# Kernel tuning notes

Hardware: AMD Instinct MI355X
Metric: run time of the kernel (lower is better)

## Reference

```python
import jax, jax.numpy as jnp
import numpy as np

GROUPS = 32
EPS = 1e-5


def group_norm(x, gamma, beta):
    # x: [b, h, w, c] NHWC; normalize over (h, w, c/GROUPS) within each group
    b, h, w, c = x.shape
    xg = x.reshape(b, h, w, GROUPS, c // GROUPS)
    mean = jnp.mean(xg, axis=(1, 2, 4), keepdims=True)
    var = jnp.var(xg, axis=(1, 2, 4), keepdims=True)
    xg = (xg - mean) * jax.lax.rsqrt(var + EPS)
    return xg.reshape(b, h, w, c) * gamma + beta


def setup_inputs() -> dict:
    key = jax.random.key(0)
    ks = jax.random.split(key, 6)
    c = 512
    s = 1.0 / np.sqrt(c)  # fan-in scaled init for conv weights
    return {
        "x": jax.random.normal(ks[0], (2, 64, 64, c), dtype=jnp.float32),
        "gamma": jnp.ones((c,), jnp.float32),
        "beta": jnp.zeros((c,), jnp.float32),
        "wq": jax.random.normal(ks[1], (c, c), jnp.float32) * s,
        "bq": jnp.zeros((c,), jnp.float32),
        "wk": jax.random.normal(ks[2], (c, c), jnp.float32) * s,
        "bk": jnp.zeros((c,), jnp.float32),
        "wv": jax.random.normal(ks[3], (c, c), jnp.float32) * s,
        "bv": jnp.zeros((c,), jnp.float32),
        "wo": jax.random.normal(ks[4], (c, c), jnp.float32) * s,
        "bo": jnp.zeros((c,), jnp.float32),
    }


def reference(x, gamma, beta, wq, bq, wk, bk, wv, bv, wo, bo):
    b, h, w, c = x.shape
    n = h * w
    hn = group_norm(x, gamma, beta)
    hn = hn.reshape(b, n, c)  # flatten spatial -> tokens
    # 1x1 convs == pointwise linear
    q = hn @ wq + bq  # [b, n, c]
    k = hn @ wk + bk
    v = hn @ wv + bv
    scores = jnp.einsum("bic,bjc->bij", q, k) * (c ** -0.5)  # [b, n, n]
    attn = jax.nn.softmax(scores, axis=-1)
    out = jnp.einsum("bij,bjc->bic", attn, v)  # [b, n, c]
    out = out @ wo + bo
    return x + out.reshape(b, h, w, c)
```

## Files before the change

### kernel.cpp

```cpp
#include <hip/hip_runtime.h>
#include <hip/hip_fp8.h>
#include <stdint.h>


typedef unsigned short u16;
typedef unsigned char u8;
typedef short s16x8 __attribute__((ext_vector_type(8)));
typedef float f32x4 __attribute__((ext_vector_type(4)));
typedef int i32x8 __attribute__((ext_vector_type(8)));
typedef float f32x16 __attribute__((ext_vector_type(16)));

#define NTOK 4096
#define CH   512

__device__ inline u16 f2bf(float f) {
  union { float f; uint32_t u; } v; v.f = f;
  uint32_t r = v.u + 0x7FFFu + ((v.u >> 16) & 1u);
  return (u16)(r >> 16);
}
__device__ inline float bf2f(u16 b) {
  union { uint32_t u; float f; } v; v.u = (uint32_t)b << 16; return v.f;
}
__device__ inline f32x4 mfma16(s16x8 a, s16x8 b, f32x4 c) {
  return __builtin_amdgcn_mfma_f32_16x16x32_bf16(a, b, c, 0, 0, 0);
}
__device__ inline f32x16 mfma_mx8(i32x8 a, i32x8 b, f32x16 c) {
  return __builtin_amdgcn_mfma_scale_f32_32x32x64_f8f6f4(
      a, b, c, 0 , 0 ,
      0, 0x7F7F7F7F, 0, 0x7F7F7F7F);
}
__device__ inline uint32_t pk_fp8x4(float e0, float e1, float e2, float e3) {
#if __has_builtin(__builtin_amdgcn_cvt_pk_fp8_f32)
  int v = __builtin_amdgcn_cvt_pk_fp8_f32(e0, e1, 0, false);
  v = __builtin_amdgcn_cvt_pk_fp8_f32(e2, e3, v, true);
  return (uint32_t)v;
#else
  __hip_fp8_e4m3 a(e0), b(e1), c(e2), d(e3);
  return (uint32_t)*(u8*)&a | ((uint32_t)*(u8*)&b << 8) |
         ((uint32_t)*(u8*)&c << 16) | ((uint32_t)*(u8*)&d << 24);
#endif
}
__device__ inline u8 f2fp8(float x) {
#if __has_builtin(__builtin_amdgcn_cvt_pk_fp8_f32)
  int v = __builtin_amdgcn_cvt_pk_fp8_f32(x, x, 0, false);
  return (u8)(v & 0xFF);
#else
  __hip_fp8_e4m3 h(x); return *(u8*)&h;
#endif
}
__device__ inline void gload_lds16(const void* g, void* l) {
  __builtin_amdgcn_global_load_lds(
      (const __attribute__((address_space(1))) unsigned*)g,
      (__attribute__((address_space(3))) unsigned*)l, 16, 0, 0);
}
__device__ inline uint4 addbf8(uint4 a, uint4 b) {
  union { uint4 v; u16 h[8]; } A, B, O; A.v = a; B.v = b;
#pragma unroll
  for (int j = 0; j < 8; j++) O.h[j] = f2bf(bf2f(A.h[j]) + bf2f(B.h[j]));
  return O.v;
}

__global__ __launch_bounds__(256) void gn_stats_kernel(
    const float* __restrict__ x, float* __restrict__ part) {
  int c = blockIdx.x, b = blockIdx.y;
  int t = threadIdx.x, g = t & 31;
  const float* xb = x + (size_t)b * NTOK * CH + (size_t)c * 64 * CH + g * 16;
  float s = 0.f, q = 0.f;
  for (int p = 0; p < 8; p++) {
    const float* ptr = xb + ((size_t)p * 8 + (t >> 5)) * CH;
#pragma unroll
    for (int j = 0; j < 4; j++) {
      float4 v = *(const float4*)(ptr + j * 4);
      s += v.x + v.y + v.z + v.w;
      q += v.x * v.x + v.y * v.y + v.z * v.z + v.w * v.w;
    }
  }
  __shared__ float ls[32][8], lq[32][8];
  ls[g][t >> 5] = s; lq[g][t >> 5] = q;
  __syncthreads();
  if (t < 32) {
    float S = 0.f, Q = 0.f;
#pragma unroll
    for (int j = 0; j < 8; j++) { S += ls[t][j]; Q += lq[t][j]; }
    float2 o; o.x = S; o.y = Q;
    *(float2*)&part[(((size_t)b * 64 + c) * 32 + t) * 2] = o;
  }
}

__global__ __launch_bounds__(256) void gn_apply_kernel(
    const float* __restrict__ x, const float* __restrict__ part,
    const float* __restrict__ gamma, const float* __restrict__ beta,
    u16* __restrict__ hn) {
  int blk = blockIdx.x, b = blk >> 9, t = threadIdx.x;
  __shared__ float msh[32], rsh[32];
  if (t < 64) {
    int g = t >> 1, half = t & 1;
    float S = 0.f, Q = 0.f;
    for (int c = half * 32; c < half * 32 + 32; c++) {
      float2 p = *(const float2*)&part[(((size_t)b * 64 + c) * 32 + g) * 2];
      S += p.x; Q += p.y;
    }
    S += __shfl_xor(S, 1, 64);
    Q += __shfl_xor(Q, 1, 64);
    if (half == 0) {
      float mean = S * (1.f / 65536.f);
      float var = Q * (1.f / 65536.f) - mean * mean;
      msh[g] = mean; rsh[g] = rsqrtf(var + 1e-5f);
    }
  }
  __syncthreads();
  size_t base = (size_t)b * NTOK * CH + (size_t)(blk & 511) * 4096 + t * 16;
  int ch0 = (t * 16) & 511;
  float mean = msh[t & 31], rstd = rsh[t & 31];
  const float* xp = x + base;
  union { u16 h[16]; uint4 v[2]; } o;
#pragma unroll
  for (int j = 0; j < 4; j++) {
    float4 xv = *(const float4*)(xp + j * 4);
    float4 gv = *(const float4*)(gamma + ch0 + j * 4);
    float4 bv = *(const float4*)(beta + ch0 + j * 4);
    o.h[j * 4 + 0] = f2bf((xv.x - mean) * rstd * gv.x + bv.x);
    o.h[j * 4 + 1] = f2bf((xv.y - mean) * rstd * gv.y + bv.y);
    o.h[j * 4 + 2] = f2bf((xv.z - mean) * rstd * gv.z + bv.z);
    o.h[j * 4 + 3] = f2bf((xv.w - mean) * rstd * gv.w + bv.w);
  }
  *(uint4*)(hn + base) = o.v[0];
  *(uint4*)(hn + base + 8) = o.v[1];
}

__global__ __launch_bounds__(256) void wprep_kernel(
    const float* w0, const float* w1, const float* w2, const float* w3,
    u16* t0, u16* t1, u16* t2, u16* t3) {
  int z = blockIdx.z;
  const float* w = z == 0 ? w0 : z == 1 ? w1 : z == 2 ? w2 : w3;
  u16* wt = z == 0 ? t0 : z == 1 ? t1 : z == 2 ? t2 : t3;
  __shared__ float tile[32][33];
  int k0 = blockIdx.x * 32, n0 = blockIdx.y * 32;
  int tx = threadIdx.x & 31, ty = threadIdx.x >> 5;
  for (int r = 0; r < 4; r++)
    tile[ty * 4 + r][tx] = w[(size_t)(k0 + ty * 4 + r) * CH + n0 + tx];
  __syncthreads();
  for (int r = 0; r < 4; r++)
    wt[(size_t)(n0 + ty * 4 + r) * CH + k0 + tx] = f2bf(tile[tx][ty * 4 + r]);
}

__global__ __launch_bounds__(256, 2) void qkv_gemm_kernel(
    const u16* __restrict__ A, const u16* __restrict__ Wcat,
    const float* __restrict__ bq, const float* __restrict__ bk,
    const float* __restrict__ bvv, u8* __restrict__ qf8, u8* __restrict__ kf8,
    u8* __restrict__ vtf8) {
  __shared__ __align__(16) u8 pool[65536];
  int m0 = blockIdx.x * 128, n0 = blockIdx.y * 128;
  int t = threadIdx.x, lane = t & 63, wave = t >> 6;
  int wx = wave & 1, wy = wave >> 1;
  int lane4 = lane >> 4;
  f32x4 acc[4][4] = {};
  const u16 *Asrc[4], *Bsrc[4];
  int dsto[4];
#pragma unroll
  for (int j = 0; j < 4; j++) {
    int u = t + j * 256, row = u >> 3, ch = (u & 7) ^ (row & 7);
    Asrc[j] = A + (size_t)(m0 + row) * CH + ch * 8;
    Bsrc[j] = Wcat + (size_t)(n0 + row) * CH + ch * 8;
    dsto[j] = u * 16;
  }
#pragma unroll
  for (int j = 0; j < 4; j++) {
    gload_lds16(Asrc[j], pool + dsto[j]);
    gload_lds16(Bsrc[j], pool + 32768 + dsto[j]);
  }
  __syncthreads();
  for (int kt = 0; kt < 8; kt++) {
    int co = (kt & 1) * 16384;
    const u16* Ac = (const u16*)(pool + co);
    const u16* Bc = (const u16*)(pool + 32768 + co);
    if (kt < 7) {
      int no = ((kt & 1) ^ 1) * 16384;
#pragma unroll
      for (int j = 0; j < 4; j++) {
        Asrc[j] += 64; Bsrc[j] += 64;
        gload_lds16(Asrc[j], pool + no + dsto[j]);
        gload_lds16(Bsrc[j], pool + 32768 + no + dsto[j]);
      }
    }
    __builtin_amdgcn_s_setprio(1);
#pragma unroll
    for (int ks = 0; ks < 2; ks++) {
      int kc = ks * 4 + lane4;
      s16x8 af[4], bf[4];
#pragma unroll
      for (int i = 0; i < 4; i++) {
        int ra = wx * 64 + i * 16 + (lane & 15);
        af[i] = *(const s16x8*)&Ac[ra * 64 + ((kc ^ (ra & 7)) << 3)];
        int rb = wy * 64 + i * 16 + (lane & 15);
        bf[i] = *(const s16x8*)&Bc[rb * 64 + ((kc ^ (rb & 7)) << 3)];
      }
#pragma unroll
      for (int mi = 0; mi < 4; mi++)
#pragma unroll
        for (int ni = 0; ni < 4; ni++)
          acc[mi][ni] = mfma16(af[mi], bf[ni], acc[mi][ni]);
    }
    __builtin_amdgcn_s_setprio(0);
    __syncthreads();
  }
  int proj = n0 >> 9;
  int r0l = wx * 64 + lane4 * 4;
  if (proj <= 1) {
    u8* O = proj == 0 ? qf8 : kf8;
    const float* bias = proj == 0 ? bq : bk;
#pragma unroll
    for (int mi = 0; mi < 4; mi++)
#pragma unroll
      for (int ni = 0; ni < 4; ni++) {
        int colp = (n0 & 511) + wy * 64 + ni * 16 + (lane & 15);
        float bv = bias[colp];
#pragma unroll
        for (int r = 0; r < 4; r++)
          O[(size_t)(m0 + r0l + mi * 16 + r) * CH + colp] =
              f2fp8(acc[mi][ni][r] + bv);
      }
  } else {
#pragma unroll
    for (int mi = 0; mi < 4; mi++)
#pragma unroll
      for (int ni = 0; ni < 4; ni++) {
        int colp = (n0 & 511) + wy * 64 + ni * 16 + (lane & 15);
        float bv = bvv[colp];
        int row = m0 + r0l + mi * 16;
        int bb = row >> 12, nn = row & 4095;
        uint32_t p = pk_fp8x4(acc[mi][ni][0] + bv, acc[mi][ni][1] + bv,
                              acc[mi][ni][2] + bv, acc[mi][ni][3] + bv);
        *(uint32_t*)&vtf8[((size_t)bb * CH + colp) * NTOK + nn] = p;
      }
  }
}

__global__ __launch_bounds__(256) void gemm_out_kernel(
    const u16* __restrict__ A, const u16* __restrict__ A2,
    const u16* __restrict__ Wt, const float* __restrict__ bias,
    float* __restrict__ out, const float* __restrict__ xres) {
  __shared__ __align__(16) u16 As[128 * 40];
  __shared__ __align__(16) u16 Bs[64 * 40];
  int m0 = blockIdx.x * 128, n0 = blockIdx.y * 64;
  int t = threadIdx.x, lane = t & 63, wave = t >> 6;
  int wm = wave >> 1, wn = wave & 1;
  f32x4 acc[4][2] = {};
  int arow = t >> 2, ac = t & 3;
  size_t aoff = (size_t)(m0 + arow) * CH + ac * 8;
  const u16* Bg = Wt + (size_t)(n0 + arow) * CH + ac * 8;
  uint4 a0 = addbf8(*(const uint4*)(A + aoff), *(const uint4*)(A2 + aoff));
  uint4 a1 = addbf8(*(const uint4*)(A + aoff + 64 * CH),
                    *(const uint4*)(A2 + aoff + 64 * CH));
  uint4 b0 = *(const uint4*)Bg;
  for (int kt = 0; kt < 16; kt++) {
    __syncthreads();
    *(uint4*)&As[(size_t)arow * 40 + ac * 8] = a0;
    *(uint4*)&As[(size_t)(arow + 64) * 40 + ac * 8] = a1;
    *(uint4*)&Bs[(size_t)arow * 40 + ac * 8] = b0;
    if (kt < 15) {
      aoff += 32; Bg += 32;
      a0 = addbf8(*(const uint4*)(A + aoff), *(const uint4*)(A2 + aoff));
      a1 = addbf8(*(const uint4*)(A + aoff + 64 * CH),
                  *(const uint4*)(A2 + aoff + 64 * CH));
      b0 = *(const uint4*)Bg;
    }
    __syncthreads();
    s16x8 af[4], bfr[2];
#pragma unroll
    for (int i = 0; i < 4; i++)
      af[i] = *(const s16x8*)&As[(wm * 64 + i * 16 + (lane & 15)) * 40 + (lane >> 4) * 8];
#pragma unroll
    for (int j = 0; j < 2; j++)
      bfr[j] = *(const s16x8*)&Bs[(wn * 32 + j * 16 + (lane & 15)) * 40 + (lane >> 4) * 8];
    __builtin_amdgcn_s_setprio(1);
#pragma unroll
    for (int mi = 0; mi < 4; mi++)
#pragma unroll
      for (int ni = 0; ni < 2; ni++)
        acc[mi][ni] = mfma16(af[mi], bfr[ni], acc[mi][ni]);
    __builtin_amdgcn_s_setprio(0);
  }
  int r0l = wm * 64 + ((lane >> 4) * 4);
  int c0l = wn * 32 + (lane & 15);
#pragma unroll
  for (int mi = 0; mi < 4; mi++)
#pragma unroll
    for (int ni = 0; ni < 2; ni++) {
      int col = n0 + c0l + ni * 16;
      float bv = bias[col];
#pragma unroll
      for (int r = 0; r < 4; r++) {
        size_t idx = (size_t)(m0 + r0l + mi * 16 + r) * CH + col;
        out[idx] = xres[idx] + acc[mi][ni][r] + bv;
      }
    }
}

__global__ __launch_bounds__(256, 2) void s_gemm_kernel(
    const u8* __restrict__ qf8, const u8* __restrict__ kf8,
    u8* __restrict__ S, float* __restrict__ lpart) {
  const float QS = 0.044194173824159216f;
  __shared__ __align__(16) u8 pool[65536];
  int bz = blockIdx.z;
  const u8* qb = qf8 + (size_t)bz * NTOK * CH;
  const u8* kb = kf8 + (size_t)bz * NTOK * CH;
  u8* Sg = S + (size_t)bz * NTOK * NTOK;
  float* lp = lpart + (size_t)bz * 64 * NTOK;
  int m0 = blockIdx.x * 128, n0 = blockIdx.y * 128;
  int t = threadIdx.x, lane = t & 63, wave = t >> 6;
  int wmx = wave & 1, wy = wave >> 1;
  int lh = lane >> 5;
  f32x16 acc[2][2] = {};
  const u8 *Asrc[4], *Bsrc[4];
  int dsto[4];
#pragma unroll
  for (int j = 0; j < 4; j++) {
    int u = t + j * 256, row = u >> 3, ch = (u & 7) ^ (row & 7);
    Asrc[j] = kb + (size_t)(n0 + row) * CH + ch * 16;
    Bsrc[j] = qb + (size_t)(m0 + row) * CH + ch * 16;
    dsto[j] = u * 16;
  }
#pragma unroll
  for (int j = 0; j < 4; j++) {
    gload_lds16(Asrc[j], pool + dsto[j]);
    gload_lds16(Bsrc[j], pool + 32768 + dsto[j]);
  }
  __syncthreads();
  for (int kt = 0; kt < 4; kt++) {
    int co = (kt & 1) * 16384;
    const u8* Ac = pool + co;
    const u8* Bc = pool + 32768 + co;
    if (kt < 3) {
      int no = ((kt & 1) ^ 1) * 16384;
#pragma unroll
      for (int j = 0; j < 4; j++) {
        Asrc[j] += 128; Bsrc[j] += 128;
        gload_lds16(Asrc[j], pool + no + dsto[j]);
        gload_lds16(Bsrc[j], pool + 32768 + no + dsto[j]);
      }
    }
    __builtin_amdgcn_s_setprio(1);
#pragma unroll
    for (int kh = 0; kh < 2; kh++) {
      int cb = kh * 4 + lh * 2;
      union { i32x8 v; uint4 qq[2]; } bu[2];
#pragma unroll
      for (int bj = 0; bj < 2; bj++) {
        int rb = wmx * 64 + bj * 32 + (lane & 31);
        const u8* bp = &Bc[rb * 128];
        bu[bj].qq[0] = *(const uint4*)&bp[(cb ^ (rb & 7)) << 4];
        bu[bj].qq[1] = *(const uint4*)&bp[((cb + 1) ^ (rb & 7)) << 4];
      }
#pragma unroll
      for (int ai = 0; ai < 2; ai++) {
        int ra = wy * 64 + ai * 32 + (lane & 31);
        union { i32x8 v; uint4 qq[2]; } au;
        const u8* ap = &Ac[ra * 128];
        au.qq[0] = *(const uint4*)&ap[(cb ^ (ra & 7)) << 4];
        au.qq[1] = *(const uint4*)&ap[((cb + 1) ^ (ra & 7)) << 4];
#pragma unroll
        for (int bj = 0; bj < 2; bj++)
          acc[ai][bj] = mfma_mx8(au.v, bu[bj].v, acc[ai][bj]);
      }
    }
    __builtin_amdgcn_s_setprio(0);
    __syncthreads();
  }
  uint32_t* Stile = (uint32_t*)pool;
  float psum[2] = {};
#pragma unroll
  for (int ai = 0; ai < 2; ai++) {
#pragma unroll
    for (int bj = 0; bj < 2; bj++) {
      int ml = wmx * 64 + bj * 32 + (lane & 31);
#pragma unroll
      for (int qd = 0; qd < 4; qd++) {
        float e0 = __expf(acc[ai][bj][qd * 4 + 0] * QS);
        float e1 = __expf(acc[ai][bj][qd * 4 + 1] * QS);
        float e2 = __expf(acc[ai][bj][qd * 4 + 2] * QS);
        float e3 = __expf(acc[ai][bj][qd * 4 + 3] * QS);
        psum[bj] += e0 + e1 + e2 + e3;
        int nw = wy * 16 + ai * 8 + qd * 2 + lh;
        Stile[ml * 32 + (nw ^ ((ml & 7) << 2))] = pk_fp8x4(e0, e1, e2, e3);
      }
    }
  }
#pragma unroll
  for (int bj = 0; bj < 2; bj++) {
    float v = psum[bj];
    v += __shfl_xor(v, 32, 64);
    if (lane < 32) {
      int m = m0 + wmx * 64 + bj * 32 + lane;
      lp[(size_t)((n0 >> 6) + wy) * NTOK + m] = v;
    }
  }
  __syncthreads();
#pragma unroll
  for (int p = 0; p < 4; p++) {
    int row = (t >> 3) + p * 32;
    int g = t & 7;
    int w0 = (g * 4) ^ ((row & 7) << 2);
    uint4 v;
    v.x = Stile[row * 32 + w0 + 0];
    v.y = Stile[row * 32 + w0 + 1];
    v.z = Stile[row * 32 + w0 + 2];
    v.w = Stile[row * 32 + w0 + 3];
    *(uint4*)&Sg[(size_t)(m0 + row) * NTOK + n0 + g * 16] = v;
  }
}

__global__ __launch_bounds__(256) void lreduce_kernel(
    const float* __restrict__ lpart, float* __restrict__ linv) {
  int b = blockIdx.y;
  int row = blockIdx.x * 256 + threadIdx.x;
  const float* lp = lpart + (size_t)b * 64 * NTOK + row;
  float s = 0.f;
#pragma unroll
  for (int c = 0; c < 64; c++) s += lp[(size_t)c * NTOK];
  linv[b * NTOK + row] = 1.f / s;
}

__global__ __launch_bounds__(512) void pv_gemm_kernel(
    const u8* __restrict__ S, const u8* __restrict__ vtf8,
    const float* __restrict__ linv, u16* __restrict__ part0,
    u16* __restrict__ part1) {
  __shared__ __align__(16) u8 Asw[2][128 * 128];
  __shared__ __align__(16) u8 Bsw[2][128 * 128];
  int flat = blockIdx.x + 32 * blockIdx.y + 128 * blockIdx.z;
  int xcd = flat & 7, u = flat >> 3;
  int m_t = xcd * 4 + (u & 3);
  int n_i = (u >> 2) & 3;
  int spb = u >> 4, sp = spb & 1, b = spb >> 1;
  int m0 = m_t * 128, n0 = n_i * 128, kbase = sp * 2048;
  const u8* Sb = S + (size_t)b * NTOK * NTOK;
  const u8* vb = vtf8 + (size_t)b * CH * NTOK;
  int t = threadIdx.x, lane = t & 63, wave = t >> 6;
  int wm = wave >> 2, wn = wave & 3;
  int lh = lane >> 5;
  f32x16 acc[2] = {};
  const u8 *Asrc[2], *Bsrc[2];
  int uoff[2];
#pragma unroll
  for (int j = 0; j < 2; j++) {
    int uu = t + j * 512, row = uu >> 3, ch = (uu & 7) ^ (row & 7);
    Asrc[j] = Sb + (size_t)(m0 + row) * NTOK + kbase + ch * 16;
    Bsrc[j] = vb + (size_t)(n0 + row) * NTOK + kbase + ch * 16;
    uoff[j] = uu * 16;
  }
#pragma unroll
  for (int j = 0; j < 2; j++) {
    gload_lds16(Asrc[j], &Asw[0][uoff[j]]); gload_lds16(Bsrc[j], &Bsw[0][uoff[j]]);
  }
  __syncthreads();
  int cur = 0;
  int rb = wn * 32 + (lane & 31);
  for (int kt = 0; kt < 16; kt++) {
    if (kt < 15) {
#pragma unroll
      for (int j = 0; j < 2; j++) {
        Asrc[j] += 128; Bsrc[j] += 128;
        gload_lds16(Asrc[j], &Asw[cur ^ 1][uoff[j]]);
        gload_lds16(Bsrc[j], &Bsw[cur ^ 1][uoff[j]]);
      }
    }
    __builtin_amdgcn_s_setprio(1);
#pragma unroll
    for (int kh = 0; kh < 2; kh++) {
      int cb = kh * 4 + lh * 2;
      union { i32x8 v; uint4 qq[2]; } bu;
      const u8* bp = &Bsw[cur][rb * 128];
      bu.qq[0] = *(const uint4*)&bp[(cb ^ (rb & 7)) << 4];
      bu.qq[1] = *(const uint4*)&bp[((cb + 1) ^ (rb & 7)) << 4];
#pragma unroll
      for (int mi = 0; mi < 2; mi++) {
        int ra = wm * 64 + mi * 32 + (lane & 31);
        union { i32x8 v; uint4 qq[2]; } au;
        const u8* ap = &Asw[cur][ra * 128];
        au.qq[0] = *(const uint4*)&ap[(cb ^ (ra & 7)) << 4];
        au.qq[1] = *(const uint4*)&ap[((cb + 1) ^ (ra & 7)) << 4];
        acc[mi] = mfma_mx8(au.v, bu.v, acc[mi]);
      }
    }
    __builtin_amdgcn_s_setprio(0);
    __syncthreads();
    cur ^= 1;
  }
  u16* Od = (sp ? part1 : part0) + (size_t)b * NTOK * CH;
  const float* lv = linv + (size_t)b * NTOK;
#pragma unroll
  for (int mi = 0; mi < 2; mi++)
#pragma unroll
    for (int reg = 0; reg < 16; reg++) {
      int crow = (reg & 3) + 8 * (reg >> 2) + 4 * lh;
      int gr = wm * 64 + mi * 32 + crow;
      float inv = lv[m0 + gr];
      Od[(size_t)(m0 + gr) * CH + n0 + wn * 32 + (lane & 31)] =
          f2bf(acc[mi][reg] * inv);
    }
}

extern "C" void kernel_launch(void* const* d_in, const int* in_sizes, int n_in,
                              void* d_out, int out_size, void* d_ws, size_t ws_size,
                              hipStream_t stream) {
  const float* x     = (const float*)d_in[0];
  const float* gamma = (const float*)d_in[1];
  const float* beta  = (const float*)d_in[2];
  const float* wq    = (const float*)d_in[3];
  const float* bq    = (const float*)d_in[4];
  const float* wk    = (const float*)d_in[5];
  const float* bk    = (const float*)d_in[6];
  const float* wv    = (const float*)d_in[7];
  const float* bv    = (const float*)d_in[8];
  const float* wo    = (const float*)d_in[9];
  const float* bo    = (const float*)d_in[10];

  char* ws = (char*)d_ws;
  u16* hn   = (u16*)(ws + 0);
  u16* q    = (u16*)(ws + 8388608);
  u8*  vtf8 = (u8*)(ws + 25165824);
  u16* wqt  = (u16*)(ws + 33554432);
  u16* wkt  = (u16*)(ws + 34078720);
  u16* wvt  = (u16*)(ws + 34603008);
  u16* wot  = (u16*)(ws + 35127296);
  u8*  S    = (u8*)(ws + 35651584);
  float* lpart = (float*)(ws + 71303168);
  float* linv  = (float*)(ws + 73400320);
  u8*  qf8  = (u8*)(ws + 75497472);
  u8*  kf8  = (u8*)(ws + 79691776);

  float* gnpart = (float*)q;

  gn_stats_kernel<<<dim3(64, 2), 256, 0, stream>>>(x, gnpart);
  wprep_kernel<<<dim3(16, 16, 4), 256, 0, stream>>>(wq, wk, wv, wo, wqt, wkt, wvt, wot);
  gn_apply_kernel<<<1024, 256, 0, stream>>>(x, gnpart, gamma, beta, hn);
  qkv_gemm_kernel<<<dim3(64, 12), 256, 0, stream>>>(hn, wqt, bq, bk, bv, qf8, kf8, vtf8);
  s_gemm_kernel<<<dim3(32, 32, 2), 256, 0, stream>>>(qf8, kf8, S, lpart);
  lreduce_kernel<<<dim3(16, 2), 256, 0, stream>>>(lpart, linv);
  pv_gemm_kernel<<<dim3(32, 4, 4), 512, 0, stream>>>(S, vtf8, linv, hn, q);
  gemm_out_kernel<<<dim3(64, 8), 256, 0, stream>>>(hn, q, wot, bo, (float*)d_out, x);
}
```

Before: 134.6 us.

## Fuse row-sum reduction into PV GEMM and use 4 waves with 2x2 tiles

Removes the separate lreduce kernel launch by having each PV GEMM block reduce the 64 partial softmax row sums for its 128 rows into shared memory before the epilogue. The PV kernel also drops from 512 threads (8 waves, 1x2 MFMA tiles each) to 256 threads (4 waves, 2x2 tiles each), raising register reuse of A/B fragments and allowing two blocks per CU. This saves a launch and a global round-trip but adds redundant sum work (each m-tile is reduced by 8 blocks) and more accumulator registers per thread.

Measured after the change: 115.2 us. -14.4%, faster.

```diff
diff --git a/kernel.cpp b/kernel.cpp
--- a/kernel.cpp
+++ b/kernel.cpp
@@ -410,23 +410,13 @@
   }
 }
 
-__global__ __launch_bounds__(256) void lreduce_kernel(
-    const float* __restrict__ lpart, float* __restrict__ linv) {
-  int b = blockIdx.y;
-  int row = blockIdx.x * 256 + threadIdx.x;
-  const float* lp = lpart + (size_t)b * 64 * NTOK + row;
-  float s = 0.f;
-#pragma unroll
-  for (int c = 0; c < 64; c++) s += lp[(size_t)c * NTOK];
-  linv[b * NTOK + row] = 1.f / s;
-}
-
-__global__ __launch_bounds__(512) void pv_gemm_kernel(
+__global__ __launch_bounds__(256, 2) void pv_gemm_kernel(
     const u8* __restrict__ S, const u8* __restrict__ vtf8,
-    const float* __restrict__ linv, u16* __restrict__ part0,
+    const float* __restrict__ lpart, u16* __restrict__ part0,
     u16* __restrict__ part1) {
-  __shared__ __align__(16) u8 Asw[2][128 * 128];
-  __shared__ __align__(16) u8 Bsw[2][128 * 128];
+  __shared__ __align__(16) u8 Asw[2][16384];
+  __shared__ __align__(16) u8 Bsw[2][16384];
+  __shared__ float linv_s[128];
   int flat = blockIdx.x + 32 * blockIdx.y + 128 * blockIdx.z;
   int xcd = flat & 7, u = flat >> 3;
   int m_t = xcd * 4 + (u & 3);
@@ -435,30 +425,31 @@
   int m0 = m_t * 128, n0 = n_i * 128, kbase = sp * 2048;
   const u8* Sb = S + (size_t)b * NTOK * NTOK;
   const u8* vb = vtf8 + (size_t)b * CH * NTOK;
+  const float* lp = lpart + (size_t)b * 64 * NTOK;
   int t = threadIdx.x, lane = t & 63, wave = t >> 6;
-  int wm = wave >> 2, wn = wave & 3;
+  int wm = wave >> 1, wn = wave & 1;
   int lh = lane >> 5;
-  f32x16 acc[2] = {};
-  const u8 *Asrc[2], *Bsrc[2];
-  int uoff[2];
-#pragma unroll
-  for (int j = 0; j < 2; j++) {
-    int uu = t + j * 512, row = uu >> 3, ch = (uu & 7) ^ (row & 7);
+  f32x16 acc[2][2] = {};
+  const u8 *Asrc[4], *Bsrc[4];
+  int uoff[4];
+#pragma unroll
+  for (int j = 0; j < 4; j++) {
+    int uu = t + j * 256, row = uu >> 3, ch = (uu & 7) ^ (row & 7);
     Asrc[j] = Sb + (size_t)(m0 + row) * NTOK + kbase + ch * 16;
     Bsrc[j] = vb + (size_t)(n0 + row) * NTOK + kbase + ch * 16;
     uoff[j] = uu * 16;
   }
 #pragma unroll
-  for (int j = 0; j < 2; j++) {
-    gload_lds16(Asrc[j], &Asw[0][uoff[j]]); gload_lds16(Bsrc[j], &Bsw[0][uoff[j]]);
+  for (int j = 0; j < 4; j++) {
+    gload_lds16(Asrc[j], &Asw[0][uoff[j]]);
+    gload_lds16(Bsrc[j], &Bsw[0][uoff[j]]);
   }
   __syncthreads();
   int cur = 0;
-  int rb = wn * 32 + (lane & 31);
   for (int kt = 0; kt < 16; kt++) {
     if (kt < 15) {
 #pragma unroll
-      for (int j = 0; j < 2; j++) {
+      for (int j = 0; j < 4; j++) {
         Asrc[j] += 128; Bsrc[j] += 128;
         gload_lds16(Asrc[j], &Asw[cur ^ 1][uoff[j]]);
         gload_lds16(Bsrc[j], &Bsw[cur ^ 1][uoff[j]]);
@@ -468,10 +459,14 @@
 #pragma unroll
     for (int kh = 0; kh < 2; kh++) {
       int cb = kh * 4 + lh * 2;
-      union { i32x8 v; uint4 qq[2]; } bu;
-      const u8* bp = &Bsw[cur][rb * 128];
-      bu.qq[0] = *(const uint4*)&bp[(cb ^ (rb & 7)) << 4];
-      bu.qq[1] = *(const uint4*)&bp[((cb + 1) ^ (rb & 7)) << 4];
+      union { i32x8 v; uint4 qq[2]; } bu[2];
+#pragma unroll
+      for (int ni = 0; ni < 2; ni++) {
+        int rb = wn * 64 + ni * 32 + (lane & 31);
+        const u8* bp = &Bsw[cur][rb * 128];
+        bu[ni].qq[0] = *(const uint4*)&bp[(cb ^ (rb & 7)) << 4];
+        bu[ni].qq[1] = *(const uint4*)&bp[((cb + 1) ^ (rb & 7)) << 4];
+      }
 #pragma unroll
       for (int mi = 0; mi < 2; mi++) {
         int ra = wm * 64 + mi * 32 + (lane & 31);
@@ -479,25 +474,34 @@
         const u8* ap = &Asw[cur][ra * 128];
         au.qq[0] = *(const uint4*)&ap[(cb ^ (ra & 7)) << 4];
         au.qq[1] = *(const uint4*)&ap[((cb + 1) ^ (ra & 7)) << 4];
-        acc[mi] = mfma_mx8(au.v, bu.v, acc[mi]);
+#pragma unroll
+        for (int ni = 0; ni < 2; ni++)
+          acc[mi][ni] = mfma_mx8(au.v, bu[ni].v, acc[mi][ni]);
       }
     }
     __builtin_amdgcn_s_setprio(0);
     __syncthreads();
     cur ^= 1;
   }
+  if (t < 128) {
+    float s = 0.f;
+#pragma unroll 8
+    for (int c = 0; c < 64; c++) s += lp[(size_t)c * NTOK + m0 + t];
+    linv_s[t] = 1.f / s;
+  }
+  __syncthreads();
   u16* Od = (sp ? part1 : part0) + (size_t)b * NTOK * CH;
-  const float* lv = linv + (size_t)b * NTOK;
 #pragma unroll
   for (int mi = 0; mi < 2; mi++)
 #pragma unroll
-    for (int reg = 0; reg < 16; reg++) {
-      int crow = (reg & 3) + 8 * (reg >> 2) + 4 * lh;
-      int gr = wm * 64 + mi * 32 + crow;
-      float inv = lv[m0 + gr];
-      Od[(size_t)(m0 + gr) * CH + n0 + wn * 32 + (lane & 31)] =
-          f2bf(acc[mi][reg] * inv);
-    }
+    for (int ni = 0; ni < 2; ni++)
+#pragma unroll
+      for (int reg = 0; reg < 16; reg++) {
+        int crow = (reg & 3) + 8 * (reg >> 2) + 4 * lh;
+        int gr = wm * 64 + mi * 32 + crow;
+        Od[(size_t)(m0 + gr) * CH + n0 + wn * 64 + ni * 32 + (lane & 31)] =
+            f2bf(acc[mi][ni][reg] * linv_s[gr]);
+      }
 }
 
 extern "C" void kernel_launch(void* const* d_in, const int* in_sizes, int n_in,
@@ -525,7 +529,6 @@
   u16* wot  = (u16*)(ws + 35127296);
   u8*  S    = (u8*)(ws + 35651584);
   float* lpart = (float*)(ws + 71303168);
-  float* linv  = (float*)(ws + 73400320);
   u8*  qf8  = (u8*)(ws + 75497472);
   u8*  kf8  = (u8*)(ws + 79691776);
 
@@ -536,7 +539,6 @@
   gn_apply_kernel<<<1024, 256, 0, stream>>>(x, gnpart, gamma, beta, hn);
   qkv_gemm_kernel<<<dim3(64, 12), 256, 0, stream>>>(hn, wqt, bq, bk, bv, qf8, kf8, vtf8);
   s_gemm_kernel<<<dim3(32, 32, 2), 256, 0, stream>>>(qf8, kf8, S, lpart);
-  lreduce_kernel<<<dim3(16, 2), 256, 0, stream>>>(lpart, linv);
-  pv_gemm_kernel<<<dim3(32, 4, 4), 512, 0, stream>>>(S, vtf8, linv, hn, q);
+  pv_gemm_kernel<<<dim3(32, 4, 4), 256, 0, stream>>>(S, vtf8, lpart, hn, q);
   gemm_out_kernel<<<dim3(64, 8), 256, 0, stream>>>(hn, q, wot, bo, (float*)d_out, x);
 }
```
